# Optimization experiments

Measured on AMD Instinct MI355X. Metric: run time of the kernel, lower is better.

## Reference

```python
import jax, jax.numpy as jnp
import numpy as np

EPS = 1e-6
GROUPS = 32  # min(C//4, 32) with C=256

def group_norm(x, scale, bias):
    B, H, W, C = x.shape
    g = GROUPS
    xg = x.reshape(B, H, W, g, C // g)
    mean = jnp.mean(xg, axis=(1, 2, 4), keepdims=True)
    var = jnp.var(xg, axis=(1, 2, 4), keepdims=True)
    xg = (xg - mean) * jax.lax.rsqrt(var + EPS)
    return xg.reshape(B, H, W, C) * scale + bias

def nin(x, w, b):
    return jnp.einsum('bhwc,cd->bhwd', x, w) + b

def setup_inputs() -> dict:
    key = jax.random.key(0)
    ks = jax.random.split(key, 11)
    B, H, W, C = 8, 64, 64, 256
    s = 1.0 / np.sqrt(C)
    return {
        'x': jax.random.normal(ks[0], (B, H, W, C), jnp.float32),
        'gn_scale': jnp.ones((C,), jnp.float32),
        'gn_bias': jnp.zeros((C,), jnp.float32),
        'Wq': jax.random.normal(ks[1], (C, C), jnp.float32) * s,
        'bq': jnp.zeros((C,), jnp.float32),
        'Wk': jax.random.normal(ks[2], (C, C), jnp.float32) * s,
        'bk': jnp.zeros((C,), jnp.float32),
        'Wv': jax.random.normal(ks[3], (C, C), jnp.float32) * s,
        'bv': jnp.zeros((C,), jnp.float32),
        'Wo': jax.random.normal(ks[4], (C, C), jnp.float32) * s * 0.1,
        'bo': jnp.zeros((C,), jnp.float32),
    }

def reference(x, gn_scale, gn_bias, Wq, bq, Wk, bk, Wv, bv, Wo, bo):
    B, H, W, C = x.shape
    h = group_norm(x, gn_scale, gn_bias)
    q = nin(h, Wq, bq)
    k = nin(h, Wk, bk)
    v = nin(h, Wv, bv)
    w = jnp.einsum('bhwc,bHWc->bhwHW', q, k) * (C ** -0.5)
    w = w.reshape(B, H, W, H * W)
    w = jax.nn.softmax(w, axis=-1)
    w = w.reshape(B, H, W, H, W)
    h = jnp.einsum('bhwHW,bHWc->bhwc', w, v)
    h = nin(h, Wo, bo)
    return x + h
```

## Files before the change

### kernel.cpp

```cpp
#include <hip/hip_runtime.h>
#include <stdint.h>

using short8 = __attribute__((ext_vector_type(8))) short;
using f32x4  = __attribute__((ext_vector_type(4))) float;

#define L2E 1.44269504088896f

static __device__ __forceinline__ unsigned short f2bf(float f) {
  union { float f; uint32_t u; } v; v.f = f;
  uint32_t r = v.u + 0x7fffu + ((v.u >> 16) & 1u);
  return (unsigned short)(r >> 16);
}
static __device__ __forceinline__ float bf2f(unsigned short u) {
  union { uint32_t u; float f; } v; v.u = ((uint32_t)u) << 16;
  return v.f;
}

static __device__ __forceinline__ void gload16(const unsigned short* g, unsigned short* l) {
  __builtin_amdgcn_global_load_lds(
      (const __attribute__((address_space(1))) void*)g,
      (__attribute__((address_space(3))) void*)l, 16, 0, 0);
}

static __device__ __forceinline__ float red_add_lg(float x) {
  x += __shfl_xor(x, 16);
  x += __shfl_xor(x, 32);
  return x;
}
static __device__ __forceinline__ float red_max_lg(float x) {
  x = fmaxf(x, __shfl_xor(x, 16));
  x = fmaxf(x, __shfl_xor(x, 32));
  return x;
}

__global__ __launch_bounds__(256) void prep_w(
    const float* __restrict__ Wq, const float* __restrict__ Wk,
    const float* __restrict__ Wv, const float* __restrict__ Wo,
    unsigned short* __restrict__ Wt) {
  int k = threadIdx.x, d = blockIdx.x, w = blockIdx.y;
  const float* src = (w==0)?Wq:(w==1)?Wk:(w==2)?Wv:Wo;
  Wt[w*65536 + d*256 + k] = f2bf(src[k*256 + d]);
}

__global__ __launch_bounds__(256) void gn_stats(
    const float* __restrict__ x, float* __restrict__ part) {
  int c = threadIdx.x, ch = blockIdx.x, b = blockIdx.y;
  float s = 0.f, q = 0.f;
  const float* p = x + ((b*4096) + ch*64)*256 + c;
  for (int it = 0; it < 64; ++it) {
    float v = p[it*256];
    s += v; q += v*v;
  }
  s += __shfl_xor(s,1); q += __shfl_xor(q,1);
  s += __shfl_xor(s,2); q += __shfl_xor(q,2);
  s += __shfl_xor(s,4); q += __shfl_xor(q,4);
  if ((c & 7) == 0) {
    int g = c >> 3;
    part[((b*64 + ch)*32 + g)*2 + 0] = s;
    part[((b*64 + ch)*32 + g)*2 + 1] = q;
  }
}

__global__ __launch_bounds__(256) void gn_apply(
    const float* __restrict__ x, const float* __restrict__ part,
    const float* __restrict__ sc, const float* __restrict__ bi,
    unsigned short* __restrict__ h) {
  int c = threadIdx.x, ch = blockIdx.x, b = blockIdx.y;
  int g = c >> 3;
  float s = 0.f, q = 0.f;
  for (int cc = 0; cc < 64; ++cc) {
    s += part[((b*64 + cc)*32 + g)*2 + 0];
    q += part[((b*64 + cc)*32 + g)*2 + 1];
  }
  float mean = s * (1.f/32768.f);
  float var  = q * (1.f/32768.f) - mean*mean;
  float rstd = rsqrtf(var + 1e-6f);
  float a  = rstd * sc[c];
  float d0 = bi[c] - mean * a;
  const float* p = x + ((b*4096) + ch*64)*256 + c;
  unsigned short* o = h + ((b*4096) + ch*64)*256 + c;
  for (int it = 0; it < 64; ++it)
    o[it*256] = f2bf(p[it*256] * a + d0);
}

__global__ __launch_bounds__(256) void gemm_bt(
    const unsigned short* __restrict__ A,
    const unsigned short* __restrict__ Bm,
    const float* __restrict__ bias_n,
    const float* __restrict__ bias_m,
    const float* __restrict__ resid,
    void* __restrict__ outp, float scale, int mode) {
  int tid = threadIdx.x;
  int w = tid >> 6, l = tid & 63, lr = l & 15, lg = l >> 4;
  int i0 = blockIdx.x * 64;
  int j0 = blockIdx.y * 256 + w * 64;
  f32x4 acc[4][4] = {};
#pragma unroll
  for (int kk = 0; kk < 8; ++kk) {
    short8 af[4], bfr[4];
#pragma unroll
    for (int mi = 0; mi < 4; ++mi)
      af[mi] = *(const short8*)(A + (i0 + mi*16 + lr)*256 + kk*32 + lg*8);
#pragma unroll
    for (int ni = 0; ni < 4; ++ni)
      bfr[ni] = *(const short8*)(Bm + (j0 + ni*16 + lr)*256 + kk*32 + lg*8);
#pragma unroll
    for (int mi = 0; mi < 4; ++mi)
#pragma unroll
      for (int ni = 0; ni < 4; ++ni)
        acc[mi][ni] = __builtin_amdgcn_mfma_f32_16x16x32_bf16(af[mi], bfr[ni], acc[mi][ni], 0,0,0);
  }
#pragma unroll
  for (int mi = 0; mi < 4; ++mi) {
#pragma unroll
    for (int ni = 0; ni < 4; ++ni) {
      int j = j0 + ni*16 + lr;
#pragma unroll
      for (int r = 0; r < 4; ++r) {
        int i = i0 + mi*16 + lg*4 + r;
        float v = acc[mi][ni][r];
        if (mode == 0) {
          ((unsigned short*)outp)[i*256 + j] = f2bf((v + bias_n[j]) * scale);
        } else if (mode == 1) {
          int idx = ((j >> 12) << 20) + i*4096 + (j & 4095);
          ((unsigned short*)outp)[idx] = f2bf(v + bias_m[i]);
        } else {
          ((float*)outp)[i*256 + j] = v + bias_n[j] + resid[i*256 + j];
        }
      }
    }
  }
}

static __device__ __forceinline__ void stage_kv32(
    const unsigned short* __restrict__ Kb, const unsigned short* __restrict__ Vb,
    int kt, unsigned short* dK, unsigned short* dV, int w, int l) {
#pragma unroll
  for (int i = 0; i < 4; ++i) {
    int t = (w*4 + i)*64 + l;
    int r = t >> 5, cs = t & 31;
    int cg = cs ^ (r & 7);
    gload16(Kb + (kt*32 + r)*256 + cg*8, dK + t*8);
  }
#pragma unroll
  for (int i = 0; i < 4; ++i) {
    int t = (w*4 + i)*64 + l;
    int d = t >> 2, s = t & 3;
    int sg = s ^ (d & 3);
    gload16(Vb + d*4096 + kt*32 + sg*8, dV + t*8);
  }
}

__global__ __launch_bounds__(256, 2) void attn_fwd(
    const unsigned short* __restrict__ Q,
    const unsigned short* __restrict__ Kmat,
    const unsigned short* __restrict__ Vt,
    unsigned short* __restrict__ P0,
    unsigned short* __restrict__ P1,
    float* __restrict__ stats) {
  __shared__ __align__(16) unsigned short ldsK[2][32][256];
  __shared__ __align__(16) unsigned short ldsV[2][256][32];

  int tid = threadIdx.x;
  int w = tid >> 6, l = tid & 63, lr = l & 15, lg = l >> 4;
  int b  = blockIdx.x & 7;
  int mt = (blockIdx.x >> 3) & 31;
  int ks = blockIdx.x >> 8;
  int m0 = mt*128 + w*32;
  int sw = lr & 7;
  int src0 = ((lg & 1) << 5) + lr;
  int src1 = src0 + 16;
  bool xsel = (lg < 2);

  const unsigned short* Kb = Kmat + b*(4096*256) + ks*(2048*256);
  const unsigned short* Vb = Vt   + (b << 20) + ks*2048;
  unsigned short* Pp = ks ? P1 : P0;

  short8 qf[2][8];
#pragma unroll
  for (int qn = 0; qn < 2; ++qn) {
    int qbase = ((b*4096) + m0 + qn*16 + lr)*256 + lg*8;
#pragma unroll
    for (int kk = 0; kk < 8; ++kk)
      qf[qn][kk] = *(const short8*)(Q + qbase + kk*32);
  }

  float mrun[2], lrun[2];
  f32x4 oacc[2][16] = {};
  mrun[0] = mrun[1] = -1e30f;
  lrun[0] = lrun[1] = 0.f;

  stage_kv32(Kb, Vb, 0, &ldsK[0][0][0], &ldsV[0][0][0], w, l);

  for (int kt = 0; kt < 64; ++kt) {
    int cur = kt & 1;
    if (kt < 63) {
      stage_kv32(Kb, Vb, kt+1, &ldsK[cur^1][0][0], &ldsV[cur^1][0][0], w, l);
      asm volatile("s_waitcnt vmcnt(8)" ::: "memory");
    } else {
      asm volatile("s_waitcnt vmcnt(0)" ::: "memory");
    }
    __builtin_amdgcn_s_barrier();
    __builtin_amdgcn_sched_barrier(0);

    const unsigned short (*Kc)[256] = ldsK[cur];
    const unsigned short (*Vc)[32]  = ldsV[cur];

    f32x4 s_[2][2];
#pragma unroll
    for (int qn = 0; qn < 2; ++qn)
#pragma unroll
      for (int kn = 0; kn < 2; ++kn) s_[qn][kn] = (f32x4){0.f,0.f,0.f,0.f};
    __builtin_amdgcn_s_setprio(1);
#pragma unroll
    for (int kn = 0; kn < 2; ++kn) {
#pragma unroll
      for (int kk = 0; kk < 8; ++kk) {
        short8 kf = *(const short8*)&Kc[kn*16 + lr][((kk*4 + lg) ^ sw)*8];
        s_[0][kn] = __builtin_amdgcn_mfma_f32_16x16x32_bf16(kf, qf[0][kk], s_[0][kn], 0,0,0);
        s_[1][kn] = __builtin_amdgcn_mfma_f32_16x16x32_bf16(kf, qf[1][kk], s_[1][kn], 0,0,0);
      }
    }
    __builtin_amdgcn_s_setprio(0);

    short8 pa[2];
#pragma unroll
    for (int qn = 0; qn < 2; ++qn) {
      float ma = fmaxf(fmaxf(s_[qn][0][0], s_[qn][0][1]), fmaxf(s_[qn][0][2], s_[qn][0][3]));
      float mb = fmaxf(fmaxf(s_[qn][1][0], s_[qn][1][1]), fmaxf(s_[qn][1][2], s_[qn][1][3]));
      float pmax = fmaxf(ma, mb);
      if (__any(pmax > mrun[qn] + 8.f)) {
        float mx = red_max_lg(pmax);
        float mnew = fmaxf(mrun[qn], mx);
        float alpha = __builtin_amdgcn_exp2f((mrun[qn] - mnew) * L2E);
        mrun[qn] = mnew;
        lrun[qn] *= alpha;
        float at[4];
#pragma unroll
        for (int r = 0; r < 4; ++r) at[r] = __shfl(alpha, lg*4 + r);
#pragma unroll
        for (int jt = 0; jt < 16; ++jt)
#pragma unroll
          for (int r = 0; r < 4; ++r) oacc[qn][jt][r] *= at[r];
      }
      float mL = mrun[qn] * L2E;
      float p[2][4];
#pragma unroll
      for (int kn = 0; kn < 2; ++kn)
#pragma unroll
        for (int r = 0; r < 4; ++r)
          p[kn][r] = __builtin_amdgcn_exp2f(s_[qn][kn][r]*L2E - mL);
      float t0 = (p[0][0]+p[0][1]) + (p[0][2]+p[0][3]);
      float t1 = (p[1][0]+p[1][1]) + (p[1][2]+p[1][3]);
      lrun[qn] += red_add_lg(t0 + t1);
      unsigned int X0, X1, Y0, Y1;
      asm("v_cvt_pk_bf16_f32 %0, %1, %2" : "=v"(X0) : "v"(p[0][0]), "v"(p[0][1]));
      asm("v_cvt_pk_bf16_f32 %0, %1, %2" : "=v"(X1) : "v"(p[0][2]), "v"(p[0][3]));
      asm("v_cvt_pk_bf16_f32 %0, %1, %2" : "=v"(Y0) : "v"(p[1][0]), "v"(p[1][1]));
      asm("v_cvt_pk_bf16_f32 %0, %1, %2" : "=v"(Y1) : "v"(p[1][2]), "v"(p[1][3]));
      unsigned int x0a = (unsigned int)__shfl((int)X0, src0);
      unsigned int x1a = (unsigned int)__shfl((int)X1, src0);
      unsigned int x0b = (unsigned int)__shfl((int)X0, src1);
      unsigned int x1b = (unsigned int)__shfl((int)X1, src1);
      unsigned int y0a = (unsigned int)__shfl((int)Y0, src0);
      unsigned int y1a = (unsigned int)__shfl((int)Y1, src0);
      unsigned int y0b = (unsigned int)__shfl((int)Y0, src1);
      unsigned int y1b = (unsigned int)__shfl((int)Y1, src1);
      union { unsigned int u[4]; short8 s8; } pk;
      pk.u[0] = xsel ? x0a : y0a;
      pk.u[1] = xsel ? x1a : y1a;
      pk.u[2] = xsel ? x0b : y0b;
      pk.u[3] = xsel ? x1b : y1b;
      pa[qn] = pk.s8;
    }

    __builtin_amdgcn_s_setprio(1);
#pragma unroll
    for (int jt = 0; jt < 16; ++jt) {
      short8 vf = *(const short8*)&Vc[jt*16 + lr][(lg ^ (lr & 3))*8];
      oacc[0][jt] = __builtin_amdgcn_mfma_f32_16x16x32_bf16(pa[0], vf, oacc[0][jt], 0,0,0);
      oacc[1][jt] = __builtin_amdgcn_mfma_f32_16x16x32_bf16(pa[1], vf, oacc[1][jt], 0,0,0);
    }
    __builtin_amdgcn_s_setprio(0);
    __builtin_amdgcn_sched_barrier(0);
    __builtin_amdgcn_s_barrier();
  }

  if (lg == 0) {
#pragma unroll
    for (int qn = 0; qn < 2; ++qn) {
      int row = b*4096 + m0 + qn*16 + lr;
      stats[(ks*32768 + row)*2 + 0] = mrun[qn];
      stats[(ks*32768 + row)*2 + 1] = lrun[qn];
    }
  }
#pragma unroll
  for (int qn = 0; qn < 2; ++qn) {
#pragma unroll
    for (int r = 0; r < 4; ++r) {
      int row = ((b*4096) + m0 + qn*16 + lg*4 + r)*256;
#pragma unroll
      for (int jt = 0; jt < 16; ++jt)
        Pp[row + jt*16 + lr] = f2bf(oacc[qn][jt][r]);
    }
  }
}

__global__ __launch_bounds__(256) void merge_attn(
    const unsigned short* __restrict__ P0,
    const unsigned short* __restrict__ P1,
    const float* __restrict__ stats,
    unsigned short* __restrict__ Out) {
  int tid = threadIdx.x;
  int row = blockIdx.x*8 + (tid >> 5);
  int c8  = (tid & 31) * 8;
  float m1 = stats[row*2 + 0],          l1 = stats[row*2 + 1];
  float m2 = stats[(32768 + row)*2 + 0], l2 = stats[(32768 + row)*2 + 1];
  float M  = fmaxf(m1, m2);
  float a1 = __builtin_amdgcn_exp2f((m1 - M) * L2E);
  float a2 = __builtin_amdgcn_exp2f((m2 - M) * L2E);
  float inv = 1.f / (a1*l1 + a2*l2);
  a1 *= inv; a2 *= inv;
  short8 v1 = *(const short8*)(P0 + row*256 + c8);
  short8 v2 = *(const short8*)(P1 + row*256 + c8);
  union { unsigned short u[8]; short8 s8; } o;
#pragma unroll
  for (int j = 0; j < 8; ++j)
    o.u[j] = f2bf(bf2f((unsigned short)v1[j])*a1 + bf2f((unsigned short)v2[j])*a2);
  *(short8*)(Out + row*256 + c8) = o.s8;
}

extern "C" void kernel_launch(void* const* d_in, const int* in_sizes, int n_in,
                              void* d_out, int out_size, void* d_ws, size_t ws_size,
                              hipStream_t stream) {
  (void)in_sizes; (void)n_in; (void)out_size; (void)ws_size;
  const float* x  = (const float*)d_in[0];
  const float* gs = (const float*)d_in[1];
  const float* gb = (const float*)d_in[2];
  const float* Wq = (const float*)d_in[3];
  const float* bq = (const float*)d_in[4];
  const float* Wk = (const float*)d_in[5];
  const float* bk = (const float*)d_in[6];
  const float* Wv = (const float*)d_in[7];
  const float* bv = (const float*)d_in[8];
  const float* Wo = (const float*)d_in[9];
  const float* bo = (const float*)d_in[10];

  char* ws = (char*)d_ws;
  unsigned short* h  = (unsigned short*)(ws);
  unsigned short* Qb = (unsigned short*)(ws + (size_t)16777216);
  unsigned short* Kb = (unsigned short*)(ws + (size_t)33554432);
  unsigned short* Vt = (unsigned short*)(ws + (size_t)50331648);
  unsigned short* Wt = (unsigned short*)(ws + (size_t)67108864);
  float* part        = (float*)(ws + (size_t)67108864 + 524288);
  float* stats       = (float*)(ws + (size_t)67108864 + 524288 + 131072);
  unsigned short* Op1 = (unsigned short*)d_out;

  prep_w  <<<dim3(256,4), 256, 0, stream>>>(Wq, Wk, Wv, Wo, Wt);
  gn_stats<<<dim3(64,8),  256, 0, stream>>>(x, part);
  gn_apply<<<dim3(64,8),  256, 0, stream>>>(x, part, gs, gb, h);
  gemm_bt<<<dim3(512,1), 256, 0, stream>>>(h, Wt,        bq, nullptr, nullptr, Qb, 0.0625f, 0);
  gemm_bt<<<dim3(512,1), 256, 0, stream>>>(h, Wt+65536,  bk, nullptr, nullptr, Kb, 1.0f,    0);
  gemm_bt<<<dim3(4,128), 256, 0, stream>>>(Wt+131072, h, nullptr, bv, nullptr, Vt, 1.0f,    1);
  attn_fwd<<<dim3(512),  256, 0, stream>>>(Qb, Kb, Vt, h, Op1, stats);
  merge_attn<<<dim3(4096), 256, 0, stream>>>(h, Op1, stats, Qb);
  gemm_bt<<<dim3(512,1), 256, 0, stream>>>(Qb, Wt+196608, bo, nullptr, x, d_out, 1.0f, 2);
}
```

Before: 350.7 us.

## Fuse Q/K projections, rework V LDS swizzle, drop attention setprio

Replaces the two separate Q and K projection GEMM launches with one kernel that reads each A tile once and computes both outputs, saving a launch and a second pass over the normalized activations. The V tile's LDS swizzle now XORs in higher row bits to spread bank accesses on the PV MFMA reads. The s_setprio hints around the attention MFMA loops are removed. The fused GEMM doubles accumulator registers (32 f32x4 per lane), which may reduce occupancy or cause spills.

```diff
diff --git a/kernel.cpp b/kernel.cpp
--- a/kernel.cpp
+++ b/kernel.cpp
@@ -81,6 +81,53 @@
   unsigned short* o = h + ((b*4096) + ch*64)*256 + c;
   for (int it = 0; it < 64; ++it)
     o[it*256] = f2bf(p[it*256] * a + d0);
+}
+
+__global__ __launch_bounds__(256) void gemm_qk(
+    const unsigned short* __restrict__ A,
+    const unsigned short* __restrict__ Wtq,
+    const unsigned short* __restrict__ Wtk,
+    const float* __restrict__ bq,
+    const float* __restrict__ bk,
+    unsigned short* __restrict__ Qout,
+    unsigned short* __restrict__ Kout) {
+  int tid = threadIdx.x;
+  int w = tid >> 6, l = tid & 63, lr = l & 15, lg = l >> 4;
+  int i0 = blockIdx.x * 64;
+  int j0 = w * 64;
+  f32x4 accq[4][4] = {}, acck[4][4] = {};
+#pragma unroll
+  for (int kk = 0; kk < 8; ++kk) {
+    short8 af[4], bfq[4], bfk[4];
+#pragma unroll
+    for (int mi = 0; mi < 4; ++mi)
+      af[mi] = *(const short8*)(A + (i0 + mi*16 + lr)*256 + kk*32 + lg*8);
+#pragma unroll
+    for (int ni = 0; ni < 4; ++ni) {
+      bfq[ni] = *(const short8*)(Wtq + (j0 + ni*16 + lr)*256 + kk*32 + lg*8);
+      bfk[ni] = *(const short8*)(Wtk + (j0 + ni*16 + lr)*256 + kk*32 + lg*8);
+    }
+#pragma unroll
+    for (int mi = 0; mi < 4; ++mi)
+#pragma unroll
+      for (int ni = 0; ni < 4; ++ni) {
+        accq[mi][ni] = __builtin_amdgcn_mfma_f32_16x16x32_bf16(af[mi], bfq[ni], accq[mi][ni], 0,0,0);
+        acck[mi][ni] = __builtin_amdgcn_mfma_f32_16x16x32_bf16(af[mi], bfk[ni], acck[mi][ni], 0,0,0);
+      }
+  }
+#pragma unroll
+  for (int mi = 0; mi < 4; ++mi) {
+#pragma unroll
+    for (int ni = 0; ni < 4; ++ni) {
+      int j = j0 + ni*16 + lr;
+#pragma unroll
+      for (int r = 0; r < 4; ++r) {
+        int i = i0 + mi*16 + lg*4 + r;
+        Qout[i*256 + j] = f2bf((accq[mi][ni][r] + bq[j]) * 0.0625f);
+        Kout[i*256 + j] = f2bf(acck[mi][ni][r] + bk[j]);
+      }
+    }
+  }
 }
 
 __global__ __launch_bounds__(256) void gemm_bt(
@@ -146,7 +193,7 @@
   for (int i = 0; i < 4; ++i) {
     int t = (w*4 + i)*64 + l;
     int d = t >> 2, s = t & 3;
-    int sg = s ^ (d & 3);
+    int sg = s ^ ((d ^ (d >> 2)) & 3);
     gload16(Vb + d*4096 + kt*32 + sg*8, dV + t*8);
   }
 }
@@ -168,6 +215,7 @@
   int ks = blockIdx.x >> 8;
   int m0 = mt*128 + w*32;
   int sw = lr & 7;
+  int vsw = (lr ^ (lr >> 2)) & 3;
   int src0 = ((lg & 1) << 5) + lr;
   int src1 = src0 + 16;
   bool xsel = (lg < 2);
@@ -211,7 +259,6 @@
     for (int qn = 0; qn < 2; ++qn)
 #pragma unroll
       for (int kn = 0; kn < 2; ++kn) s_[qn][kn] = (f32x4){0.f,0.f,0.f,0.f};
-    __builtin_amdgcn_s_setprio(1);
 #pragma unroll
     for (int kn = 0; kn < 2; ++kn) {
 #pragma unroll
@@ -221,7 +268,6 @@
         s_[1][kn] = __builtin_amdgcn_mfma_f32_16x16x32_bf16(kf, qf[1][kk], s_[1][kn], 0,0,0);
       }
     }
-    __builtin_amdgcn_s_setprio(0);
 
     short8 pa[2];
 #pragma unroll
@@ -274,14 +320,12 @@
       pa[qn] = pk.s8;
     }
 
-    __builtin_amdgcn_s_setprio(1);
 #pragma unroll
     for (int jt = 0; jt < 16; ++jt) {
-      short8 vf = *(const short8*)&Vc[jt*16 + lr][(lg ^ (lr & 3))*8];
+      short8 vf = *(const short8*)&Vc[jt*16 + lr][(lg ^ vsw)*8];
       oacc[0][jt] = __builtin_amdgcn_mfma_f32_16x16x32_bf16(pa[0], vf, oacc[0][jt], 0,0,0);
       oacc[1][jt] = __builtin_amdgcn_mfma_f32_16x16x32_bf16(pa[1], vf, oacc[1][jt], 0,0,0);
     }
-    __builtin_amdgcn_s_setprio(0);
     __builtin_amdgcn_sched_barrier(0);
     __builtin_amdgcn_s_barrier();
   }
@@ -359,9 +403,8 @@
   prep_w  <<<dim3(256,4), 256, 0, stream>>>(Wq, Wk, Wv, Wo, Wt);
   gn_stats<<<dim3(64,8),  256, 0, stream>>>(x, part);
   gn_apply<<<dim3(64,8),  256, 0, stream>>>(x, part, gs, gb, h);
-  gemm_bt<<<dim3(512,1), 256, 0, stream>>>(h, Wt,        bq, nullptr, nullptr, Qb, 0.0625f, 0);
-  gemm_bt<<<dim3(512,1), 256, 0, stream>>>(h, Wt+65536,  bk, nullptr, nullptr, Kb, 1.0f,    0);
-  gemm_bt<<<dim3(4,128), 256, 0, stream>>>(Wt+131072, h, nullptr, bv, nullptr, Vt, 1.0f,    1);
+  gemm_qk<<<dim3(512,1), 256, 0, stream>>>(h, Wt, Wt+65536, bq, bk, Qb, Kb);
+  gemm_bt<<<dim3(4,128), 256, 0, stream>>>(Wt+131072, h, nullptr, bv, nullptr, Vt, 1.0f, 1);
   attn_fwd<<<dim3(512),  256, 0, stream>>>(Qb, Kb, Vt, h, Op1, stats);
   merge_attn<<<dim3(4096), 256, 0, stream>>>(h, Op1, stats, Qb);
   gemm_bt<<<dim3(512,1), 256, 0, stream>>>(Qb, Wt+196608, bo, nullptr, x, d_out, 1.0f, 2);
```

Result: faster. 327.8 us (-6.5%).
